# Optimization experiments

Measured on AMD Instinct MI355X. Metric: run time of the kernel, lower is better.

Reference implementation:

```python
import jax, jax.numpy as jnp
import numpy as np

BETA = 0.25


def setup_inputs() -> dict:
    key = jax.random.key(0)
    k1, k2 = jax.random.split(key)
    inputs = jax.random.normal(k1, (16, 64, 64, 256), dtype=jnp.float32)
    # codebook, shape (embedding_dim=256, num_embeddings=1024), uniform init like tf
    embeddings = jax.random.uniform(k2, (256, 1024), dtype=jnp.float32)
    return {"inputs": inputs, "embeddings": embeddings}


def reference(inputs, embeddings):
    D = embeddings.shape[0]
    flat = inputs.reshape(-1, D)  # [N, D]
    distances = (
        jnp.sum(flat * flat, axis=1, keepdims=True)
        - 2.0 * (flat @ embeddings)
        + jnp.sum(embeddings * embeddings, axis=0, keepdims=True)
    )
    encoding_indices = jnp.argmin(distances, axis=1)  # == argmax(-d)
    # one_hot @ embeddings.T is just a row gather from the codebook
    quantized = jnp.take(embeddings.T, encoding_indices, axis=0).reshape(inputs.shape)
    commitment_loss = BETA * jnp.mean(
        (jax.lax.stop_gradient(quantized) - inputs) ** 2
    )
    # straight-through estimator
    quantized = inputs + jax.lax.stop_gradient(quantized - inputs)
    return quantized, commitment_loss, encoding_indices
```

## Files before the change

kernel.cpp:

```cpp
#include <hip/hip_runtime.h>
#include <float.h>

typedef _Float16 half8 __attribute__((ext_vector_type(8)));
typedef float    f32x4 __attribute__((ext_vector_type(4)));

#define N_ROWS   65536
#define DIM      256
#define KCODES   1024
#define VQ_BETA  0.25
#define MARGIN   1.5f
#define HCAP     640

__global__ void transpose_e(const float* __restrict__ E, float* __restrict__ Et) {
    __shared__ float t[32][33];
    const int kt = blockIdx.x * 32;
    const int dt = blockIdx.y * 32;
    const int lx = threadIdx.x & 31;
    const int ly = threadIdx.x >> 5;
#pragma unroll
    for (int i = 0; i < 4; ++i) {
        int d = dt + ly + i * 8;
        t[ly + i * 8][lx] = E[(size_t)d * KCODES + kt + lx];
    }
    __syncthreads();
#pragma unroll
    for (int i = 0; i < 4; ++i) {
        int k = kt + ly + i * 8;
        Et[(size_t)k * DIM + dt + lx] = t[lx][ly + i * 8];
    }
}

__global__ void enorm_kernel(const float* __restrict__ E, float* __restrict__ enorm) {
    const int k = blockIdx.x * 256 + threadIdx.x;
    float s = 0.f;
#pragma unroll 4
    for (int d = 0; d < DIM; ++d) {
        float v = E[(size_t)d * KCODES + k];
        s = fmaf(v, v, s);
    }
    enorm[k] = s;
}

__global__ void efrag_kernel(const float* __restrict__ Et, _Float16* __restrict__ Efb) {
    const int fid = blockIdx.x * 256 + threadIdx.x;
    const int lhi   = fid & 3;
    const int llo   = (fid >> 2) & 15;
    const int nt    = (fid >> 6) & 3;
    const int w     = (fid >> 8) & 3;
    const int slice = fid >> 10;
    const int chunk = slice >> 3, ks = slice & 7;
    const int code  = chunk * 256 + w * 64 + nt * 16 + llo;
    const float* src = Et + (size_t)code * DIM + ks * 32 + lhi * 8;
    half8 h;
#pragma unroll
    for (int j = 0; j < 8; ++j) h[j] = (_Float16)src[j];
    *reinterpret_cast<half8*>(Efb + (size_t)fid * 8) = h;
}

__device__ __forceinline__ void load_bf(const _Float16* __restrict__ eb,
                                        half8 (&bf)[4]) {
    bf[0] = *reinterpret_cast<const half8*>(eb);
    bf[1] = *reinterpret_cast<const half8*>(eb + 512);
    bf[2] = *reinterpret_cast<const half8*>(eb + 1024);
    bf[3] = *reinterpret_cast<const half8*>(eb + 1536);
}
__device__ __forceinline__ void load_af(const char* AhB, int ks, int llo, int lhi,
                                        int aswz, half8 (&af)[4]) {
#pragma unroll
    for (int mt = 0; mt < 4; ++mt) {
        const int addr = ((mt * 16 + llo) * 512 + (ks * 4 + lhi) * 16) ^ aswz;
        af[mt] = *reinterpret_cast<const half8*>(AhB + addr);
    }
}
__device__ __forceinline__ void mfma16(const half8 (&af)[4], const half8 (&bf)[4],
                                       f32x4 (&acc)[4][4]) {
#pragma unroll
    for (int mt = 0; mt < 4; ++mt)
#pragma unroll
        for (int nt = 0; nt < 4; ++nt)
            acc[mt][nt] = __builtin_amdgcn_mfma_f32_16x16x32_f16(
                af[mt], bf[nt], acc[mt][nt], 0, 0, 0);
}
__device__ __forceinline__ void mfma_chunk(
        const _Float16* __restrict__ ebase, const char* AhB,
        int llo, int lhi, int aswz, f32x4 (&acc)[4][4]) {
    half8 bfa[4], bfb[4], af[4];
    load_bf(ebase, bfa);
#pragma unroll
    for (int ks2 = 0; ks2 < 4; ++ks2) {
        const int ksA = ks2 * 2, ksB = ks2 * 2 + 1;
        load_bf(ebase + (size_t)ksB * 8192, bfb);
        load_af(AhB, ksA, llo, lhi, aswz, af);
        mfma16(af, bfa, acc);
        if (ksB < 7) load_bf(ebase + (size_t)(ksB + 1) * 8192, bfa);
        load_af(AhB, ksB, llo, lhi, aswz, af);
        mfma16(af, bfb, acc);
    }
}

__global__ __launch_bounds__(256, 2) void vq_mfma(
        const float* __restrict__ X, const _Float16* __restrict__ Efb,
        const float* __restrict__ enorm, const float* __restrict__ Et,
        float* __restrict__ outidx, float* __restrict__ outq,
        float* __restrict__ partials)
{
    __shared__ _Float16 Ah[64 * 256];
    __shared__ float    bminw[4][64];
    __shared__ float    cutoff_s[64];
    __shared__ float    rmin_s[64];
    __shared__ unsigned minb[64], mini[64];
    __shared__ int      rowbad[64];
    __shared__ int      hits[HCAP];
    __shared__ float    dstore[HCAP];
    __shared__ unsigned hitcnt;

    const int tid = threadIdx.x;
    const int rowbase = blockIdx.x * 64;

    if (tid == 0) hitcnt = 0;
    if (tid < 64) {
        minb[tid] = 0xFFFFFFFFu; mini[tid] = 0xFFFFFFFFu;
        rmin_s[tid] = FLT_MAX;   rowbad[tid] = 0;
    }

    {
        const int row = tid >> 2;
#pragma unroll
        for (int i = 0; i < 8; ++i) {
            const int g = (tid & 3) + 4 * i;
            const float* src = X + (size_t)(rowbase + row) * DIM + g * 8;
            float4 a = *reinterpret_cast<const float4*>(src);
            float4 b = *reinterpret_cast<const float4*>(src + 4);
            half8 h;
            h[0] = (_Float16)a.x; h[1] = (_Float16)a.y;
            h[2] = (_Float16)a.z; h[3] = (_Float16)a.w;
            h[4] = (_Float16)b.x; h[5] = (_Float16)b.y;
            h[6] = (_Float16)b.z; h[7] = (_Float16)b.w;
            const int addr = (row * 512 + g * 16) ^ ((row & 7) << 4);
            *reinterpret_cast<half8*>(reinterpret_cast<char*>(Ah) + addr) = h;
        }
    }
    __syncthreads();

    const int w    = tid >> 6;
    const int lane = tid & 63;
    const int lhi  = lane >> 4, llo = lane & 15;
    const int aswz = (llo & 7) << 4;
    const int lane_off8 = (llo * 4 + lhi) * 8;
    const char* AhB = reinterpret_cast<const char*>(Ah);

    for (int chunk = 0; chunk < 4; ++chunk) {
        f32x4 acc[4][4];
#pragma unroll
        for (int mt = 0; mt < 4; ++mt)
#pragma unroll
            for (int nt = 0; nt < 4; ++nt) acc[mt][nt] = (f32x4){0.f, 0.f, 0.f, 0.f};

        const _Float16* ebase = Efb + (size_t)chunk * 65536 + w * 2048 + lane_off8;
        mfma_chunk(ebase, AhB, llo, lhi, aswz, acc);

        float e2v[4];
#pragma unroll
        for (int nt = 0; nt < 4; ++nt)
            e2v[nt] = enorm[chunk * 256 + w * 64 + nt * 16 + llo];

        float mloc[16];
#pragma unroll
        for (int mt = 0; mt < 4; ++mt)
#pragma unroll
            for (int q = 0; q < 4; ++q) {
                float m = FLT_MAX;
#pragma unroll
                for (int nt = 0; nt < 4; ++nt) {
                    const float ds = fmaf(-2.0f, acc[mt][nt][q], e2v[nt]);
                    acc[mt][nt][q] = ds;
                    m = fminf(m, ds);
                }
                mloc[mt * 4 + q] = m;
            }
#pragma unroll
        for (int m = 1; m < 16; m <<= 1)
#pragma unroll
            for (int sl = 0; sl < 16; ++sl)
                mloc[sl] = fminf(mloc[sl], __shfl_xor(mloc[sl], m, 64));
        if (llo == 0) {
#pragma unroll
            for (int mt = 0; mt < 4; ++mt)
#pragma unroll
                for (int q = 0; q < 4; ++q)
                    bminw[w][mt * 16 + lhi * 4 + q] = mloc[mt * 4 + q];
        }
        __syncthreads();
        if (tid < 64) {
            float r = fminf(fminf(bminw[0][tid], bminw[1][tid]),
                            fminf(bminw[2][tid], bminw[3][tid]));
            r = fminf(rmin_s[tid], r);
            rmin_s[tid]   = r;
            cutoff_s[tid] = r + MARGIN;
        }
        __syncthreads();

#pragma unroll
        for (int mt = 0; mt < 4; ++mt)
#pragma unroll
            for (int q = 0; q < 4; ++q) {
                const int row = mt * 16 + lhi * 4 + q;
                const float cut = cutoff_s[row];
#pragma unroll
                for (int nt = 0; nt < 4; ++nt) {
                    if (acc[mt][nt][q] < cut) {
                        const unsigned p = atomicAdd(&hitcnt, 1u);
                        if (p < HCAP)
                            hits[p] = (row << 10) |
                                      (chunk * 256 + w * 64 + nt * 16 + llo);
                        else
                            rowbad[row] = 1;
                    }
                }
            }
    }
    __syncthreads();

    const int nh = (int)(hitcnt < HCAP ? hitcnt : (unsigned)HCAP);

    for (int hi = tid; hi < nh; hi += 256) {
        const int pk = hits[hi];
        const int rl = pk >> 10, code = pk & 1023;
        const float* xr = X  + (size_t)(rowbase + rl) * DIM;
        const float* er = Et + (size_t)code * DIM;
        float p = 0.f, x2 = 0.f;
#pragma unroll
        for (int j = 0; j < 64; ++j) {
            float4 xv = *reinterpret_cast<const float4*>(xr + j * 4);
            float4 ev = *reinterpret_cast<const float4*>(er + j * 4);
            x2 = fmaf(xv.x, xv.x, x2); x2 = fmaf(xv.y, xv.y, x2);
            x2 = fmaf(xv.z, xv.z, x2); x2 = fmaf(xv.w, xv.w, x2);
            p  = fmaf(xv.x, ev.x, p);  p  = fmaf(xv.y, ev.y, p);
            p  = fmaf(xv.z, ev.z, p);  p  = fmaf(xv.w, ev.w, p);
        }
        const float dd = (x2 - 2.0f * p) + enorm[code];
        dstore[hi] = dd;
        atomicMin(&minb[rl], __float_as_uint(dd));
    }
    __syncthreads();
    for (int hi = tid; hi < nh; hi += 256) {
        const int pk = hits[hi];
        const int rl = pk >> 10;
        if (__float_as_uint(dstore[hi]) == minb[rl])
            atomicMin(&mini[rl], (unsigned)(pk & 1023));
    }
    __syncthreads();

    float* xs = dstore;
    for (int r = 0; r < 64; ++r) {
        if (!rowbad[r]) continue;
        xs[tid] = X[(size_t)(rowbase + r) * DIM + tid];
        __syncthreads();
        float x2 = 0.f;
        for (int d = 0; d < DIM; ++d) x2 = fmaf(xs[d], xs[d], x2);
        float a0 = 0.f, a1 = 0.f, a2 = 0.f, a3 = 0.f;
        const float* e0 = Et + (size_t)(tid      ) * DIM;
        const float* e1 = Et + (size_t)(tid + 256) * DIM;
        const float* e2p = Et + (size_t)(tid + 512) * DIM;
        const float* e3 = Et + (size_t)(tid + 768) * DIM;
        for (int d = 0; d < DIM; ++d) {
            const float xv = xs[d];
            a0 = fmaf(xv, e0[d], a0);
            a1 = fmaf(xv, e1[d], a1);
            a2 = fmaf(xv, e2p[d], a2);
            a3 = fmaf(xv, e3[d], a3);
        }
        const float d0 = (x2 - 2.0f * a0) + enorm[tid];
        const float d1 = (x2 - 2.0f * a1) + enorm[tid + 256];
        const float d2 = (x2 - 2.0f * a2) + enorm[tid + 512];
        const float d3 = (x2 - 2.0f * a3) + enorm[tid + 768];
        atomicMin(&minb[r], __float_as_uint(d0));
        atomicMin(&minb[r], __float_as_uint(d1));
        atomicMin(&minb[r], __float_as_uint(d2));
        atomicMin(&minb[r], __float_as_uint(d3));
        __syncthreads();
        const unsigned mb = minb[r];
        if (__float_as_uint(d0) == mb) atomicMin(&mini[r], (unsigned)tid);
        if (__float_as_uint(d1) == mb) atomicMin(&mini[r], (unsigned)(tid + 256));
        if (__float_as_uint(d2) == mb) atomicMin(&mini[r], (unsigned)(tid + 512));
        if (__float_as_uint(d3) == mb) atomicMin(&mini[r], (unsigned)(tid + 768));
        __syncthreads();
    }

    float* red = dstore;
    {
        const int row  = tid >> 2;
        const int part = tid & 3;
        const int cw   = (int)mini[row];
        const float* xrow = X  + (size_t)(rowbase + row) * DIM;
        const float* ew   = Et + (size_t)cw * DIM;
        float* oq = outq + (size_t)(rowbase + row) * DIM;
        if (part == 0) outidx[rowbase + row] = (float)cw;

        float lsum = 0.f;
#pragma unroll
        for (int j = 0; j < 16; ++j) {
            const int d0 = j * 16 + part * 4;
            float4 q = *reinterpret_cast<const float4*>(ew + d0);
            float4 x = *reinterpret_cast<const float4*>(xrow + d0);
            float4 o;
            o.x = x.x + (q.x - x.x);
            o.y = x.y + (q.y - x.y);
            o.z = x.z + (q.z - x.z);
            o.w = x.w + (q.w - x.w);
            *reinterpret_cast<float4*>(oq + d0) = o;
            float dx;
            dx = q.x - x.x; lsum = fmaf(dx, dx, lsum);
            dx = q.y - x.y; lsum = fmaf(dx, dx, lsum);
            dx = q.z - x.z; lsum = fmaf(dx, dx, lsum);
            dx = q.w - x.w; lsum = fmaf(dx, dx, lsum);
        }
        __syncthreads();
        red[tid] = lsum;
    }
    __syncthreads();
    for (int s = 128; s > 0; s >>= 1) {
        if (tid < s) red[tid] += red[tid + s];
        __syncthreads();
    }
    if (tid == 0) partials[blockIdx.x] = red[0];
}

__global__ void loss_final(const float* __restrict__ partials, float* __restrict__ out) {
    __shared__ double sd[256];
    const int tid = threadIdx.x;
    double s = 0.0;
    for (int i = tid; i < 1024; i += 256) s += (double)partials[i];
    sd[tid] = s;
    __syncthreads();
    for (int k = 128; k > 0; k >>= 1) {
        if (tid < k) sd[tid] += sd[tid + k];
        __syncthreads();
    }
    if (tid == 0) out[0] = (float)(VQ_BETA * sd[0] / (double)((size_t)N_ROWS * DIM));
}

extern "C" void kernel_launch(void* const* d_in, const int* in_sizes, int n_in,
                              void* d_out, int out_size, void* d_ws, size_t ws_size,
                              hipStream_t stream) {
    const float* X = (const float*)d_in[0];
    const float* E = (const float*)d_in[1];

    float* outq    = (float*)d_out;
    float* outloss = outq + (size_t)N_ROWS * DIM;
    float* outidx  = outloss + 1;

    float*    Et       = (float*)d_ws;
    _Float16* Efb      = (_Float16*)(Et + 262144);
    float*    enormw   = (float*)(Efb + 262144);
    float*    partials = enormw + KCODES;

    transpose_e <<<dim3(32, 8), 256, 0, stream>>>(E, Et);
    enorm_kernel<<<4,           256, 0, stream>>>(E, enormw);
    efrag_kernel<<<128,         256, 0, stream>>>(Et, Efb);
    vq_mfma     <<<N_ROWS / 64, 256, 0, stream>>>(X, Efb, enormw, Et,
                                                  outidx, outq, partials);
    loss_final  <<<1,           256, 0, stream>>>(partials, outloss);
}
```

Measured before the change: 172.7 us.

## Fix pruning cutoff from first chunk and pack distance-index into 64-bit atomic min

```diff
diff --git a/kernel.cpp b/kernel.cpp
--- a/kernel.cpp
+++ b/kernel.cpp
@@ -3,6 +3,7 @@
 
 typedef _Float16 half8 __attribute__((ext_vector_type(8)));
 typedef float    f32x4 __attribute__((ext_vector_type(4)));
+typedef unsigned long long u64;
 
 #define N_ROWS   65536
 #define DIM      256
@@ -10,6 +11,11 @@
 #define VQ_BETA  0.25
 #define MARGIN   1.5f
 #define HCAP     640
+
+__device__ __forceinline__ unsigned fkey(float f) {
+    const unsigned u = __float_as_uint(f);
+    return u ^ (0x80000000u | (unsigned)((int)u >> 31));
+}
 
 __global__ void transpose_e(const float* __restrict__ E, float* __restrict__ Et) {
     __shared__ float t[32][33];
@@ -57,8 +63,8 @@
     *reinterpret_cast<half8*>(Efb + (size_t)fid * 8) = h;
 }
 
-__device__ __forceinline__ void load_bf(const _Float16* __restrict__ eb,
-                                        half8 (&bf)[4]) {
+__device__ __forceinline__ void load_bf4(const _Float16* __restrict__ eb,
+                                         half8 (&bf)[4]) {
     bf[0] = *reinterpret_cast<const half8*>(eb);
     bf[1] = *reinterpret_cast<const half8*>(eb + 512);
     bf[2] = *reinterpret_cast<const half8*>(eb + 1024);
@@ -85,14 +91,14 @@
         const _Float16* __restrict__ ebase, const char* AhB,
         int llo, int lhi, int aswz, f32x4 (&acc)[4][4]) {
     half8 bfa[4], bfb[4], af[4];
-    load_bf(ebase, bfa);
+    load_bf4(ebase, bfa);
 #pragma unroll
     for (int ks2 = 0; ks2 < 4; ++ks2) {
         const int ksA = ks2 * 2, ksB = ks2 * 2 + 1;
-        load_bf(ebase + (size_t)ksB * 8192, bfb);
+        load_bf4(ebase + (size_t)ksB * 8192, bfb);
         load_af(AhB, ksA, llo, lhi, aswz, af);
         mfma16(af, bfa, acc);
-        if (ksB < 7) load_bf(ebase + (size_t)(ksB + 1) * 8192, bfa);
+        if (ksB < 7) load_bf4(ebase + (size_t)(ksB + 1) * 8192, bfa);
         load_af(AhB, ksB, llo, lhi, aswz, af);
         mfma16(af, bfb, acc);
     }
@@ -107,11 +113,11 @@
     __shared__ _Float16 Ah[64 * 256];
     __shared__ float    bminw[4][64];
     __shared__ float    cutoff_s[64];
-    __shared__ float    rmin_s[64];
-    __shared__ unsigned minb[64], mini[64];
+    __shared__ u64      minpk[64];
     __shared__ int      rowbad[64];
     __shared__ int      hits[HCAP];
-    __shared__ float    dstore[HCAP];
+    __shared__ float    xs[DIM];
+    __shared__ float    wlsum[4];
     __shared__ unsigned hitcnt;
 
     const int tid = threadIdx.x;
@@ -119,8 +125,8 @@
 
     if (tid == 0) hitcnt = 0;
     if (tid < 64) {
-        minb[tid] = 0xFFFFFFFFu; mini[tid] = 0xFFFFFFFFu;
-        rmin_s[tid] = FLT_MAX;   rowbad[tid] = 0;
+        minpk[tid] = 0xFFFFFFFFFFFFFFFFULL;
+        rowbad[tid] = 0;
     }
 
     {
@@ -149,20 +155,20 @@
     const int lane_off8 = (llo * 4 + lhi) * 8;
     const char* AhB = reinterpret_cast<const char*>(Ah);
 
-    for (int chunk = 0; chunk < 4; ++chunk) {
+    {
         f32x4 acc[4][4];
 #pragma unroll
         for (int mt = 0; mt < 4; ++mt)
 #pragma unroll
             for (int nt = 0; nt < 4; ++nt) acc[mt][nt] = (f32x4){0.f, 0.f, 0.f, 0.f};
 
-        const _Float16* ebase = Efb + (size_t)chunk * 65536 + w * 2048 + lane_off8;
+        float e2v[4];
+#pragma unroll
+        for (int nt = 0; nt < 4; ++nt)
+            e2v[nt] = enorm[w * 64 + nt * 16 + llo];
+
+        const _Float16* ebase = Efb + w * 2048 + lane_off8;
         mfma_chunk(ebase, AhB, llo, lhi, aswz, acc);
-
-        float e2v[4];
-#pragma unroll
-        for (int nt = 0; nt < 4; ++nt)
-            e2v[nt] = enorm[chunk * 256 + w * 64 + nt * 16 + llo];
 
         float mloc[16];
 #pragma unroll
@@ -194,8 +200,6 @@
         if (tid < 64) {
             float r = fminf(fminf(bminw[0][tid], bminw[1][tid]),
                             fminf(bminw[2][tid], bminw[3][tid]));
-            r = fminf(rmin_s[tid], r);
-            rmin_s[tid]   = r;
             cutoff_s[tid] = r + MARGIN;
         }
         __syncthreads();
@@ -205,10 +209,46 @@
 #pragma unroll
             for (int q = 0; q < 4; ++q) {
                 const int row = mt * 16 + lhi * 4 + q;
-                const float cut = cutoff_s[row];
+                const float c = cutoff_s[row];
 #pragma unroll
                 for (int nt = 0; nt < 4; ++nt) {
-                    if (acc[mt][nt][q] < cut) {
+                    if (acc[mt][nt][q] < c) {
+                        const unsigned p = atomicAdd(&hitcnt, 1u);
+                        if (p < HCAP)
+                            hits[p] = (row << 10) | (w * 64 + nt * 16 + llo);
+                        else
+                            rowbad[row] = 1;
+                    }
+                }
+            }
+    }
+
+#pragma unroll 1
+    for (int chunk = 1; chunk < 4; ++chunk) {
+        f32x4 acc[4][4];
+#pragma unroll
+        for (int mt = 0; mt < 4; ++mt)
+#pragma unroll
+            for (int nt = 0; nt < 4; ++nt) acc[mt][nt] = (f32x4){0.f, 0.f, 0.f, 0.f};
+
+        float e2v[4];
+#pragma unroll
+        for (int nt = 0; nt < 4; ++nt)
+            e2v[nt] = enorm[chunk * 256 + w * 64 + nt * 16 + llo];
+
+        const _Float16* ebase = Efb + (size_t)chunk * 65536 + w * 2048 + lane_off8;
+        mfma_chunk(ebase, AhB, llo, lhi, aswz, acc);
+
+#pragma unroll
+        for (int mt = 0; mt < 4; ++mt)
+#pragma unroll
+            for (int q = 0; q < 4; ++q) {
+                const int row = mt * 16 + lhi * 4 + q;
+                const float c = cutoff_s[row];
+#pragma unroll
+                for (int nt = 0; nt < 4; ++nt) {
+                    const float ds = fmaf(-2.0f, acc[mt][nt][q], e2v[nt]);
+                    if (ds < c) {
                         const unsigned p = atomicAdd(&hitcnt, 1u);
                         if (p < HCAP)
                             hits[p] = (row << 10) |
@@ -218,6 +258,7 @@
                     }
                 }
             }
+        __builtin_amdgcn_sched_barrier(0);
     }
     __syncthreads();
 
@@ -239,65 +280,51 @@
             p  = fmaf(xv.z, ev.z, p);  p  = fmaf(xv.w, ev.w, p);
         }
         const float dd = (x2 - 2.0f * p) + enorm[code];
-        dstore[hi] = dd;
-        atomicMin(&minb[rl], __float_as_uint(dd));
-    }
-    __syncthreads();
-    for (int hi = tid; hi < nh; hi += 256) {
-        const int pk = hits[hi];
-        const int rl = pk >> 10;
-        if (__float_as_uint(dstore[hi]) == minb[rl])
-            atomicMin(&mini[rl], (unsigned)(pk & 1023));
-    }
-    __syncthreads();
-
-    float* xs = dstore;
+        atomicMin(&minpk[rl], ((u64)fkey(dd) << 10) | (unsigned)code);
+    }
+    __syncthreads();
+
     for (int r = 0; r < 64; ++r) {
         if (!rowbad[r]) continue;
         xs[tid] = X[(size_t)(rowbase + r) * DIM + tid];
         __syncthreads();
-        float x2 = 0.f;
-        for (int d = 0; d < DIM; ++d) x2 = fmaf(xs[d], xs[d], x2);
-        float a0 = 0.f, a1 = 0.f, a2 = 0.f, a3 = 0.f;
-        const float* e0 = Et + (size_t)(tid      ) * DIM;
-        const float* e1 = Et + (size_t)(tid + 256) * DIM;
-        const float* e2p = Et + (size_t)(tid + 512) * DIM;
-        const float* e3 = Et + (size_t)(tid + 768) * DIM;
-        for (int d = 0; d < DIM; ++d) {
-            const float xv = xs[d];
-            a0 = fmaf(xv, e0[d], a0);
-            a1 = fmaf(xv, e1[d], a1);
-            a2 = fmaf(xv, e2p[d], a2);
-            a3 = fmaf(xv, e3[d], a3);
-        }
-        const float d0 = (x2 - 2.0f * a0) + enorm[tid];
-        const float d1 = (x2 - 2.0f * a1) + enorm[tid + 256];
-        const float d2 = (x2 - 2.0f * a2) + enorm[tid + 512];
-        const float d3 = (x2 - 2.0f * a3) + enorm[tid + 768];
-        atomicMin(&minb[r], __float_as_uint(d0));
-        atomicMin(&minb[r], __float_as_uint(d1));
-        atomicMin(&minb[r], __float_as_uint(d2));
-        atomicMin(&minb[r], __float_as_uint(d3));
-        __syncthreads();
-        const unsigned mb = minb[r];
-        if (__float_as_uint(d0) == mb) atomicMin(&mini[r], (unsigned)tid);
-        if (__float_as_uint(d1) == mb) atomicMin(&mini[r], (unsigned)(tid + 256));
-        if (__float_as_uint(d2) == mb) atomicMin(&mini[r], (unsigned)(tid + 512));
-        if (__float_as_uint(d3) == mb) atomicMin(&mini[r], (unsigned)(tid + 768));
-        __syncthreads();
-    }
-
-    float* red = dstore;
+        {
+            float x2 = 0.f;
+            for (int d = 0; d < DIM; ++d) x2 = fmaf(xs[d], xs[d], x2);
+            float a0 = 0.f, a1 = 0.f, a2 = 0.f, a3 = 0.f;
+            const float* e0 = Et + (size_t)(tid      ) * DIM;
+            const float* e1 = Et + (size_t)(tid + 256) * DIM;
+            const float* e2p = Et + (size_t)(tid + 512) * DIM;
+            const float* e3 = Et + (size_t)(tid + 768) * DIM;
+            for (int d = 0; d < DIM; ++d) {
+                const float xv = xs[d];
+                a0 = fmaf(xv, e0[d], a0);
+                a1 = fmaf(xv, e1[d], a1);
+                a2 = fmaf(xv, e2p[d], a2);
+                a3 = fmaf(xv, e3[d], a3);
+            }
+            const float d0 = (x2 - 2.0f * a0) + enorm[tid];
+            const float d1 = (x2 - 2.0f * a1) + enorm[tid + 256];
+            const float d2 = (x2 - 2.0f * a2) + enorm[tid + 512];
+            const float d3 = (x2 - 2.0f * a3) + enorm[tid + 768];
+            atomicMin(&minpk[r], ((u64)fkey(d0) << 10) | (unsigned)tid);
+            atomicMin(&minpk[r], ((u64)fkey(d1) << 10) | (unsigned)(tid + 256));
+            atomicMin(&minpk[r], ((u64)fkey(d2) << 10) | (unsigned)(tid + 512));
+            atomicMin(&minpk[r], ((u64)fkey(d3) << 10) | (unsigned)(tid + 768));
+        }
+        __syncthreads();
+    }
+
+    float lsum = 0.f;
     {
         const int row  = tid >> 2;
         const int part = tid & 3;
-        const int cw   = (int)mini[row];
+        const int cw   = (int)(minpk[row] & 1023ULL);
         const float* xrow = X  + (size_t)(rowbase + row) * DIM;
         const float* ew   = Et + (size_t)cw * DIM;
         float* oq = outq + (size_t)(rowbase + row) * DIM;
         if (part == 0) outidx[rowbase + row] = (float)cw;
 
-        float lsum = 0.f;
 #pragma unroll
         for (int j = 0; j < 16; ++j) {
             const int d0 = j * 16 + part * 4;
@@ -315,15 +342,15 @@
             dx = q.z - x.z; lsum = fmaf(dx, dx, lsum);
             dx = q.w - x.w; lsum = fmaf(dx, dx, lsum);
         }
-        __syncthreads();
-        red[tid] = lsum;
-    }
-    __syncthreads();
-    for (int s = 128; s > 0; s >>= 1) {
-        if (tid < s) red[tid] += red[tid + s];
-        __syncthreads();
-    }
-    if (tid == 0) partials[blockIdx.x] = red[0];
+    }
+#pragma unroll
+    for (int m = 1; m < 64; m <<= 1) lsum += __shfl_xor(lsum, m, 64);
+    if (lane == 0) wlsum[w] = lsum;
+    __syncthreads();
+    if (tid == 0) {
+        float s = wlsum[0] + wlsum[1] + wlsum[2] + wlsum[3];
+        partials[blockIdx.x] = s;
+    }
 }
 
 __global__ void loss_final(const float* __restrict__ partials, float* __restrict__ out) {
```

Result: slower. 196.0 us (+13.5%).
